# Optimization experiments

Hardware: AMD Instinct MI355X
Metric: run time of the kernel (lower is better)

Reference implementation:

```python
import jax, jax.numpy as jnp
import numpy as np

N_NODES = 50000
N_EDGES = 800000
IN_FEATS = 128
HIDDEN = 128
NUM_CLASSES = 47


def setup_inputs() -> dict:
    key = jax.random.key(0)
    k1, k2, k3, k4 = jax.random.split(key, 4)
    features = jax.random.normal(k1, (N_NODES, IN_FEATS), dtype=jnp.float32)
    edge_index = jax.random.randint(k2, (2, N_EDGES), 0, N_NODES, dtype=jnp.int32)
    # Glorot-style init for weights, zeros for bias (DGL GraphConv defaults)
    W1 = jax.random.normal(k3, (IN_FEATS, HIDDEN), dtype=jnp.float32) * (1.0 / np.sqrt(IN_FEATS))
    b1 = jnp.zeros((HIDDEN,), dtype=jnp.float32)
    W2 = jax.random.normal(k4, (HIDDEN, NUM_CLASSES), dtype=jnp.float32) * (1.0 / np.sqrt(HIDDEN))
    b2 = jnp.zeros((NUM_CLASSES,), dtype=jnp.float32)
    return {"features": features, "edge_index": edge_index,
            "W1": W1, "b1": b1, "W2": W2, "b2": b2}


def _graph_conv(x, W, b, src, dst, norm_src, norm_dst, n_nodes):
    # DGL GraphConv, norm='both': D_dst^{-1/2} A D_src^{-1/2} (X W) + b
    h = (x * norm_src[:, None]) @ W            # transform before aggregation
    agg = jax.ops.segment_sum(h[src], dst, num_segments=n_nodes)
    return agg * norm_dst[:, None] + b


def reference(features, edge_index, W1, b1, W2, b2):
    src, dst = edge_index[0], edge_index[1]
    n = features.shape[0]
    ones = jnp.ones((src.shape[0],), dtype=features.dtype)
    deg_out = jax.ops.segment_sum(ones, src, num_segments=n)
    deg_in = jax.ops.segment_sum(ones, dst, num_segments=n)
    norm_src = jax.lax.rsqrt(jnp.clip(deg_out, 1.0))   # d_out^{-1/2}, clamp >= 1
    norm_dst = jax.lax.rsqrt(jnp.clip(deg_in, 1.0))    # d_in^{-1/2}, clamp >= 1

    h = _graph_conv(features, W1, b1, src, dst, norm_src, norm_dst, n)
    h = jax.nn.relu(h)
    out = _graph_conv(h, W2, b2, src, dst, norm_src, norm_dst, n)
    return out
```

## Files before the change

kernel.cpp:

```cpp
#include <hip/hip_runtime.h>
#include <hip/hip_fp16.h>

#define N_NODES 50000
#define N_EDGES 800000
#define IN_F 128
#define HID 128
#define NCLS 47
#define H2S 48
#define W2C 64
#define NCH 196
#define NB 128
#define CHUNK 6250
#define PDW 12500
#define G1ROWS 256
#define G2ROWS 128


typedef _Float16 f16x8 __attribute__((ext_vector_type(8)));
typedef float f32x4 __attribute__((ext_vector_type(4)));

struct __align__(8)  h2x2 { __half2 a, b; };
struct __align__(16) h2x4 { __half2 a, b, c, d; };

__global__ __launch_bounds__(256) void prep_kernel(const float* __restrict__ W1,
                                                   const float* __restrict__ W2,
                                                   __half* __restrict__ W1Th,
                                                   __half* __restrict__ W1Tl,
                                                   __half* __restrict__ W2Th,
                                                   __half* __restrict__ W2Tl) {
    const int b = blockIdx.x, t = threadIdx.x;
    if (b < 32) {
        const int i0 = b * 512;
        for (int i2 = i0 + t; i2 < i0 + 512; i2 += 256) {
            int cc = i2 >> 7, k = i2 & 127;
            float w = W1[k * HID + cc];
            __half hv = __float2half_rn(w);
            W1Th[i2] = hv;
            W1Tl[i2] = __float2half_rn(w - __half2float(hv));
        }
    } else {
        const int i0 = (b - 32) * 512;
        for (int i2 = i0 + t; i2 < i0 + 512; i2 += 256) {
            int cc = i2 >> 7, k = i2 & 127;
            float w = (cc < NCLS) ? W2[k * NCLS + cc] : 0.f;
            __half hv = __float2half_rn(w);
            W2Th[i2] = hv;
            W2Tl[i2] = __float2half_rn(w - __half2float(hv));
        }
    }
}

__global__ __launch_bounds__(512) void hist_gemm1_kernel(const int* __restrict__ ei,
        unsigned int* __restrict__ Pdst, unsigned int* __restrict__ Psrc,
        const float* __restrict__ X, const __half* __restrict__ W1Th,
        const __half* __restrict__ W1Tl, __half* __restrict__ H1h) {
    __shared__ unsigned int h[PDW];
    const int t = threadIdx.x;
    if (blockIdx.x < 2 * NB) {
        const bool is_src = blockIdx.x >= NB;
        const int chunk = blockIdx.x & (NB - 1);
        const int* ids = is_src ? ei : ei + N_EDGES;
        uint2* h2 = (uint2*)h;
        for (int j = t; j < PDW / 2; j += 512) h2[j] = make_uint2(0u, 0u);
        __syncthreads();
        const int e0 = chunk * CHUNK;
        const int2* e2p = (const int2*)(ids + e0);
        for (int k = t; k < CHUNK / 2; k += 512) {
            int2 v2 = e2p[k];
            atomicAdd(&h[v2.x >> 2], 1u << ((v2.x & 3) * 8));
            atomicAdd(&h[v2.y >> 2], 1u << ((v2.y & 3) * 8));
        }
        __syncthreads();
        unsigned int* P = (is_src ? Psrc : Pdst) + (size_t)chunk * PDW;
        uint2* P2 = (uint2*)P;
        for (int j = t; j < PDW / 2; j += 512) P2[j] = h2[j];
    } else {
        const int lane = t & 63;
        const int wv = t >> 6;
        const int r16 = lane & 15;
        const int kg = lane >> 4;
        const int row0 = (blockIdx.x - 2 * NB) * G1ROWS + wv * 32;
        f32x4 acc[2][8] = {};
#pragma unroll
        for (int s = 0; s < 4; ++s) {
            const int k0 = 32 * s + 8 * kg;
            f16x8 ah[2], al[2];
#pragma unroll
            for (int rt = 0; rt < 2; ++rt) {
                int row = row0 + rt * 16 + r16;
                int rc = row < N_NODES ? row : N_NODES - 1;
                const float4 x0 = *(const float4*)&X[(size_t)rc * IN_F + k0];
                const float4 x1 = *(const float4*)&X[(size_t)rc * IN_F + k0 + 4];
                const float xv[8] = {x0.x, x0.y, x0.z, x0.w,
                                     x1.x, x1.y, x1.z, x1.w};
#pragma unroll
                for (int j = 0; j < 8; ++j) {
                    _Float16 hv = (_Float16)xv[j];
                    ah[rt][j] = hv;
                    al[rt][j] = (_Float16)(xv[j] - (float)hv);
                }
            }
#pragma unroll
            for (int tt = 0; tt < 8; ++tt) {
                const f16x8 bh = *(const f16x8*)&W1Th[(16 * tt + r16) * IN_F + k0];
                const f16x8 bl = *(const f16x8*)&W1Tl[(16 * tt + r16) * IN_F + k0];
#pragma unroll
                for (int rt = 0; rt < 2; ++rt) {
                    acc[rt][tt] = __builtin_amdgcn_mfma_f32_16x16x32_f16(
                        ah[rt], bh, acc[rt][tt], 0, 0, 0);
                    acc[rt][tt] = __builtin_amdgcn_mfma_f32_16x16x32_f16(
                        al[rt], bh, acc[rt][tt], 0, 0, 0);
                    acc[rt][tt] = __builtin_amdgcn_mfma_f32_16x16x32_f16(
                        ah[rt], bl, acc[rt][tt], 0, 0, 0);
                }
            }
        }
#pragma unroll
        for (int rt = 0; rt < 2; ++rt)
#pragma unroll
            for (int j = 0; j < 4; ++j) {
                const int row = row0 + rt * 16 + 4 * kg + j;
                if (row < N_NODES) {
#pragma unroll
                    for (int tt = 0; tt < 8; ++tt)
                        H1h[(size_t)row * HID + 16 * tt + r16] =
                            __float2half_rn(acc[rt][tt][j]);
                }
            }
    }
}

__global__ __launch_bounds__(256) void reduce_kernel(unsigned int* __restrict__ Pdst,
                                                     const unsigned int* __restrict__ Psrc,
                                                     int* __restrict__ cnt_in,
                                                     float* __restrict__ norm_src,
                                                     float* __restrict__ norm_dst,
                                                     int* __restrict__ chunk_sums) {
    __shared__ int sm[256];
    const int t = threadIdx.x;
    const int j = blockIdx.x * 256 + t;
    int tot = 0;
    if (j < PDW) {
        unsigned int run = 0;
#pragma unroll 8
        for (int b = 0; b < NB; ++b) {
            unsigned int v = Pdst[(size_t)b * PDW + j];
            Pdst[(size_t)b * PDW + j] = run;
            run += v;
        }
        int n0 = run & 0xff, n1 = (run >> 8) & 0xff;
        int n2 = (run >> 16) & 0xff, n3 = (run >> 24) & 0xff;
        *(int4*)&cnt_in[4 * j] = make_int4(n0, n1, n2, n3);
        *(float4*)&norm_dst[4 * j] = make_float4(
            rsqrtf(fmaxf((float)n0, 1.0f)), rsqrtf(fmaxf((float)n1, 1.0f)),
            rsqrtf(fmaxf((float)n2, 1.0f)), rsqrtf(fmaxf((float)n3, 1.0f)));
        tot = n0 + n1 + n2 + n3;
        unsigned int rs = 0;
#pragma unroll 8
        for (int b = 0; b < NB; ++b) rs += Psrc[(size_t)b * PDW + j];
        int s0 = rs & 0xff, s1 = (rs >> 8) & 0xff;
        int s2 = (rs >> 16) & 0xff, s3 = (rs >> 24) & 0xff;
        *(float4*)&norm_src[4 * j] = make_float4(
            rsqrtf(fmaxf((float)s0, 1.0f)), rsqrtf(fmaxf((float)s1, 1.0f)),
            rsqrtf(fmaxf((float)s2, 1.0f)), rsqrtf(fmaxf((float)s3, 1.0f)));
    }
    sm[t] = tot;
    __syncthreads();
    const int g = t & 63;
    for (int off = 32; off > 0; off >>= 1) {
        if (g < off) sm[t] += sm[t + off];
        __syncthreads();
    }
    if (g == 0) chunk_sums[blockIdx.x * 4 + (t >> 6)] = sm[t];
}

__global__ __launch_bounds__(256) void scan3_kernel(const int* __restrict__ cnt_in,
                                                    const int* __restrict__ chunk_sums,
                                                    int* __restrict__ offsets) {
    __shared__ int sm[256];
    const int t = threadIdx.x;
    int v = (t < NCH) ? chunk_sums[t] : 0;
    sm[t] = v;
    __syncthreads();
    for (int off = 1; off < 256; off <<= 1) {
        int u = (t >= off) ? sm[t - off] : 0;
        __syncthreads();
        sm[t] += u;
        __syncthreads();
    }
    const int basev = (blockIdx.x == 0) ? 0 : sm[blockIdx.x - 1];
    __syncthreads();
    const int idx = blockIdx.x * 256 + t;
    int c = (idx < N_NODES) ? cnt_in[idx] : 0;
    sm[t] = c;
    __syncthreads();
    for (int off = 1; off < 256; off <<= 1) {
        int u = (t >= off) ? sm[t - off] : 0;
        __syncthreads();
        sm[t] += u;
        __syncthreads();
    }
    if (idx < N_NODES) offsets[idx] = basev + sm[t] - c;
    if (blockIdx.x == 0 && t == 0) offsets[N_NODES] = N_EDGES;
}

__global__ __launch_bounds__(512) void fill_kernel(const int* __restrict__ src,
        const int* __restrict__ dst, const int* __restrict__ offsets,
        const unsigned int* __restrict__ Pdst, int* __restrict__ csr_src) {
    __shared__ __align__(16) unsigned int cur[PDW];
    const int t = threadIdx.x;
    const int chunk = blockIdx.x;
    uint2* c2 = (uint2*)cur;
    for (int j = t; j < PDW / 2; j += 512) c2[j] = make_uint2(0u, 0u);
    __syncthreads();
    const unsigned int* base = Pdst + (size_t)chunk * PDW;
    const int e0 = chunk * CHUNK;
    const int2* d2p = (const int2*)(dst + e0);
    const int2* s2p = (const int2*)(src + e0);
    for (int k = t; k < CHUNK / 2; k += 512) {
        int2 d2 = d2p[k];
        int2 s2 = s2p[k];
        {
            const int d = d2.x;
            const int sh = (d & 3) * 8;
            const unsigned int bw = base[d >> 2];
            const int off = offsets[d];
            unsigned int old = atomicAdd(&cur[d >> 2], 1u << sh);
            csr_src[off + (int)((bw >> sh) & 0xffu) + (int)((old >> sh) & 0xffu)] = s2.x;
        }
        {
            const int d = d2.y;
            const int sh = (d & 3) * 8;
            const unsigned int bw = base[d >> 2];
            const int off = offsets[d];
            unsigned int old = atomicAdd(&cur[d >> 2], 1u << sh);
            csr_src[off + (int)((bw >> sh) & 0xffu) + (int)((old >> sh) & 0xffu)] = s2.y;
        }
    }
}

__global__ __launch_bounds__(256) void gather1_kernel(const __half* __restrict__ H1h,
        const int* __restrict__ offsets, const int* __restrict__ csr_src,
        const float* __restrict__ b1, const float* __restrict__ norm_src,
        const float* __restrict__ norm_dst, __half* __restrict__ Hrelu16) {
    const int lane = threadIdx.x & 63;
    const int q = lane >> 4;
    const int fl = lane & 15;
    const int row = blockIdx.x * 4 + (threadIdx.x >> 6);
    const int beg = offsets[row], end = offsets[row + 1];
    float a0 = 0.f, a1 = 0.f, a2 = 0.f, a3 = 0.f;
    float a4 = 0.f, a5 = 0.f, a6 = 0.f, a7 = 0.f;
    for (int base = beg; base < end; base += 64) {
        int idx = 0;
        float nsv = 0.f;
        if (base + lane < end) {
            idx = csr_src[base + lane];
            nsv = norm_src[idx];
        }
        const int cnt = min(end - base, 64);
        for (int j = 0; j < cnt; j += 16) {
            int e0 = j + q, e1 = j + 4 + q, e2 = j + 8 + q, e3 = j + 12 + q;
            int s0 = __shfl(idx, e0);  float n0 = __shfl(nsv, e0);
            int s1 = __shfl(idx, e1);  float n1 = __shfl(nsv, e1);
            int s2 = __shfl(idx, e2);  float n2 = __shfl(nsv, e2);
            int s3 = __shfl(idx, e3);  float n3 = __shfl(nsv, e3);
            h2x4 v0 = *(const h2x4*)&H1h[(size_t)s0 * HID + 8 * fl];
            h2x4 v1 = *(const h2x4*)&H1h[(size_t)s1 * HID + 8 * fl];
            h2x4 v2 = *(const h2x4*)&H1h[(size_t)s2 * HID + 8 * fl];
            h2x4 v3 = *(const h2x4*)&H1h[(size_t)s3 * HID + 8 * fl];
            float2 f;
            f = __half22float2(v0.a); a0 = fmaf(f.x, n0, a0); a1 = fmaf(f.y, n0, a1);
            f = __half22float2(v0.b); a2 = fmaf(f.x, n0, a2); a3 = fmaf(f.y, n0, a3);
            f = __half22float2(v0.c); a4 = fmaf(f.x, n0, a4); a5 = fmaf(f.y, n0, a5);
            f = __half22float2(v0.d); a6 = fmaf(f.x, n0, a6); a7 = fmaf(f.y, n0, a7);
            f = __half22float2(v1.a); a0 = fmaf(f.x, n1, a0); a1 = fmaf(f.y, n1, a1);
            f = __half22float2(v1.b); a2 = fmaf(f.x, n1, a2); a3 = fmaf(f.y, n1, a3);
            f = __half22float2(v1.c); a4 = fmaf(f.x, n1, a4); a5 = fmaf(f.y, n1, a5);
            f = __half22float2(v1.d); a6 = fmaf(f.x, n1, a6); a7 = fmaf(f.y, n1, a7);
            f = __half22float2(v2.a); a0 = fmaf(f.x, n2, a0); a1 = fmaf(f.y, n2, a1);
            f = __half22float2(v2.b); a2 = fmaf(f.x, n2, a2); a3 = fmaf(f.y, n2, a3);
            f = __half22float2(v2.c); a4 = fmaf(f.x, n2, a4); a5 = fmaf(f.y, n2, a5);
            f = __half22float2(v2.d); a6 = fmaf(f.x, n2, a6); a7 = fmaf(f.y, n2, a7);
            f = __half22float2(v3.a); a0 = fmaf(f.x, n3, a0); a1 = fmaf(f.y, n3, a1);
            f = __half22float2(v3.b); a2 = fmaf(f.x, n3, a2); a3 = fmaf(f.y, n3, a3);
            f = __half22float2(v3.c); a4 = fmaf(f.x, n3, a4); a5 = fmaf(f.y, n3, a5);
            f = __half22float2(v3.d); a6 = fmaf(f.x, n3, a6); a7 = fmaf(f.y, n3, a7);
        }
    }
    a0 += __shfl_xor(a0, 16); a1 += __shfl_xor(a1, 16);
    a2 += __shfl_xor(a2, 16); a3 += __shfl_xor(a3, 16);
    a4 += __shfl_xor(a4, 16); a5 += __shfl_xor(a5, 16);
    a6 += __shfl_xor(a6, 16); a7 += __shfl_xor(a7, 16);
    a0 += __shfl_xor(a0, 32); a1 += __shfl_xor(a1, 32);
    a2 += __shfl_xor(a2, 32); a3 += __shfl_xor(a3, 32);
    a4 += __shfl_xor(a4, 32); a5 += __shfl_xor(a5, 32);
    a6 += __shfl_xor(a6, 32); a7 += __shfl_xor(a7, 32);
    if (lane < 16) {
        float nd = norm_dst[row], ns = norm_src[row];
        float4 bA = *(const float4*)&b1[8 * fl];
        float4 bB = *(const float4*)&b1[8 * fl + 4];
        float o0 = fmaxf(fmaf(a0, nd, bA.x), 0.f) * ns;
        float o1 = fmaxf(fmaf(a1, nd, bA.y), 0.f) * ns;
        float o2 = fmaxf(fmaf(a2, nd, bA.z), 0.f) * ns;
        float o3 = fmaxf(fmaf(a3, nd, bA.w), 0.f) * ns;
        float o4 = fmaxf(fmaf(a4, nd, bB.x), 0.f) * ns;
        float o5 = fmaxf(fmaf(a5, nd, bB.y), 0.f) * ns;
        float o6 = fmaxf(fmaf(a6, nd, bB.z), 0.f) * ns;
        float o7 = fmaxf(fmaf(a7, nd, bB.w), 0.f) * ns;
        h2x4 p = {__floats2half2_rn(o0, o1), __floats2half2_rn(o2, o3),
                  __floats2half2_rn(o4, o5), __floats2half2_rn(o6, o7)};
        *(h2x4*)&Hrelu16[(size_t)row * HID + 8 * fl] = p;
    }
}

__global__ __launch_bounds__(256) void gemm2_kernel(const __half* __restrict__ Hrelu16,
                                                    const __half* __restrict__ W2Th,
                                                    const __half* __restrict__ W2Tl,
                                                    __half* __restrict__ H2h) {
    const int lane = threadIdx.x & 63;
    const int wv = threadIdx.x >> 6;
    const int r16 = lane & 15;
    const int kg = lane >> 4;
    const int row0 = blockIdx.x * G2ROWS + wv * 32;
    f32x4 acc[2][3] = {};
#pragma unroll
    for (int s = 0; s < 4; ++s) {
        const int k0 = 32 * s + 8 * kg;
        f16x8 a[2];
#pragma unroll
        for (int rt = 0; rt < 2; ++rt) {
            int row = row0 + rt * 16 + r16;
            int rc = row < N_NODES ? row : N_NODES - 1;
            a[rt] = *(const f16x8*)&Hrelu16[(size_t)rc * HID + k0];
        }
#pragma unroll
        for (int tt = 0; tt < 3; ++tt) {
            const f16x8 bh = *(const f16x8*)&W2Th[(16 * tt + r16) * HID + k0];
            const f16x8 bl = *(const f16x8*)&W2Tl[(16 * tt + r16) * HID + k0];
#pragma unroll
            for (int rt = 0; rt < 2; ++rt) {
                acc[rt][tt] = __builtin_amdgcn_mfma_f32_16x16x32_f16(
                    a[rt], bh, acc[rt][tt], 0, 0, 0);
                acc[rt][tt] = __builtin_amdgcn_mfma_f32_16x16x32_f16(
                    a[rt], bl, acc[rt][tt], 0, 0, 0);
            }
        }
    }
#pragma unroll
    for (int rt = 0; rt < 2; ++rt)
#pragma unroll
        for (int j = 0; j < 4; ++j) {
            const int row = row0 + rt * 16 + 4 * kg + j;
            if (row < N_NODES) {
#pragma unroll
                for (int tt = 0; tt < 3; ++tt)
                    H2h[(size_t)row * H2S + 16 * tt + r16] =
                        __float2half_rn(acc[rt][tt][j]);
            }
        }
}

__global__ __launch_bounds__(256) void gather2_kernel(const __half* __restrict__ H2h,
        const int* __restrict__ offsets, const int* __restrict__ csr_src,
        const float* __restrict__ b2, const float* __restrict__ norm_dst,
        float* __restrict__ out) {
    const int lane = threadIdx.x & 63;
    const int row = blockIdx.x * 4 + (threadIdx.x >> 6);
    const int beg = offsets[row], end = offsets[row + 1];
    const int cl = min(lane, H2S - 1);
    float acc = 0.f;
    for (int base = beg; base < end; base += 64) {
        int idx = 0;
        float wv = 0.f;
        if (base + lane < end) {
            idx = csr_src[base + lane];
            wv = 1.f;
        }
        const int cnt = min(end - base, 64);
        for (int j = 0; j < cnt; j += 4) {
            int s0 = __shfl(idx, j);     float w0 = __shfl(wv, j);
            int s1 = __shfl(idx, j + 1); float w1 = __shfl(wv, j + 1);
            int s2 = __shfl(idx, j + 2); float w2 = __shfl(wv, j + 2);
            int s3 = __shfl(idx, j + 3); float w3 = __shfl(wv, j + 3);
            float f0 = __half2float(H2h[(size_t)s0 * H2S + cl]);
            float f1 = __half2float(H2h[(size_t)s1 * H2S + cl]);
            float f2 = __half2float(H2h[(size_t)s2 * H2S + cl]);
            float f3 = __half2float(H2h[(size_t)s3 * H2S + cl]);
            acc = fmaf(f0, w0, acc);
            acc = fmaf(f1, w1, acc);
            acc = fmaf(f2, w2, acc);
            acc = fmaf(f3, w3, acc);
        }
    }
    if (lane < NCLS) out[(size_t)row * NCLS + lane] = acc * norm_dst[row] + b2[lane];
}

extern "C" void kernel_launch(void* const* d_in, const int* in_sizes, int n_in,
                              void* d_out, int out_size, void* d_ws, size_t ws_size,
                              hipStream_t stream) {
    const float* X  = (const float*)d_in[0];
    const int*   ei = (const int*)d_in[1];
    const float* W1 = (const float*)d_in[2];
    const float* b1 = (const float*)d_in[3];
    const float* W2 = (const float*)d_in[4];
    const float* b2 = (const float*)d_in[5];
    float* out = (float*)d_out;

    const int* src = ei;
    const int* dst = ei + N_EDGES;

    char* w = (char*)d_ws;
    auto alloc = [&](size_t bytes) {
        char* p = w;
        w += (bytes + 255) & ~(size_t)255;
        return p;
    };
    float*  norm_src   = (float*)alloc(N_NODES * 4);
    float*  norm_dst   = (float*)alloc(N_NODES * 4);
    int*    cnt_in     = (int*)alloc(N_NODES * 4);
    int*    offsets    = (int*)alloc((N_NODES + 1) * 4);
    int*    csr_src    = (int*)alloc((size_t)N_EDGES * 4);
    int*    chunk_sums = (int*)alloc(NCH * 4);
    __half* W1Th       = (__half*)alloc((size_t)IN_F * HID * 2);
    __half* W1Tl       = (__half*)alloc((size_t)IN_F * HID * 2);
    __half* W2Th       = (__half*)alloc((size_t)W2C * HID * 2);
    __half* W2Tl       = (__half*)alloc((size_t)W2C * HID * 2);
    __half* H1h        = (__half*)alloc((size_t)N_NODES * HID * 2);
    __half* Hrelu16    = (__half*)alloc((size_t)N_NODES * HID * 2);
    __half* H2h        = (__half*)alloc((size_t)N_NODES * H2S * 2);
    unsigned int* Pdst = (unsigned int*)alloc((size_t)NB * PDW * 4);
    unsigned int* Psrc = (unsigned int*)alloc((size_t)NB * PDW * 4);

    const int g1_blocks = (N_NODES + G1ROWS - 1) / G1ROWS;
    const int g2_blocks = (N_NODES + G2ROWS - 1) / G2ROWS;
    prep_kernel<<<48, 256, 0, stream>>>(W1, W2, W1Th, W1Tl, W2Th, W2Tl);
    hist_gemm1_kernel<<<2 * NB + g1_blocks, 512, 0, stream>>>(ei, Pdst, Psrc,
                                                              X, W1Th, W1Tl, H1h);
    reduce_kernel<<<(PDW + 255) / 256, 256, 0, stream>>>(Pdst, Psrc, cnt_in,
                                                         norm_src, norm_dst, chunk_sums);
    scan3_kernel<<<NCH, 256, 0, stream>>>(cnt_in, chunk_sums, offsets);
    fill_kernel<<<NB, 512, 0, stream>>>(src, dst, offsets, Pdst, csr_src);
    gather1_kernel<<<N_NODES / 4, 256, 0, stream>>>(H1h, offsets, csr_src, b1,
                                                    norm_src, norm_dst, Hrelu16);
    gemm2_kernel<<<g2_blocks, 256, 0, stream>>>(Hrelu16, W2Th, W2Tl, H2h);
    gather2_kernel<<<N_NODES / 4, 256, 0, stream>>>(H2h, offsets, csr_src, b2,
                                                    norm_dst, out);
}
```

Baseline: 207.2 us.

## Fuse all pipeline stages into one cooperative persistent kernel with grid syncs

Replaces the eight separate kernel launches with a single cooperative mega-kernel that runs each stage as a grid-strided job loop, separated by grid.sync(). The aim is to remove per-launch overhead and inter-kernel gaps. The grid is capped at 512 blocks of 512 threads, so stages that used to launch tens of thousands of small blocks now loop. It also moves the gemm1 stage after the histogram stage, so the two no longer overlap. The trade-offs are grid-wide barrier cost, parallelism limited by occupancy, and the 50KB LDS array shared by every stage, which may limit blocks per CU.

```diff
diff --git a/kernel.cpp b/kernel.cpp
--- a/kernel.cpp
+++ b/kernel.cpp
@@ -1,5 +1,8 @@
 #include <hip/hip_runtime.h>
 #include <hip/hip_fp16.h>
+#include <hip/hip_cooperative_groups.h>
+
+namespace cg = cooperative_groups;
 
 #define N_NODES 50000
 #define N_EDGES 800000
@@ -13,7 +16,9 @@
 #define CHUNK 6250
 #define PDW 12500
 #define G1ROWS 256
-#define G2ROWS 128
+#define G2ROWS 256
+#define NTHR 512
+#define MAXG 512
 
 
 typedef _Float16 f16x8 __attribute__((ext_vector_type(8)));
@@ -22,96 +27,333 @@
 struct __align__(8)  h2x2 { __half2 a, b; };
 struct __align__(16) h2x4 { __half2 a, b, c, d; };
 
-__global__ __launch_bounds__(256) void prep_kernel(const float* __restrict__ W1,
-                                                   const float* __restrict__ W2,
-                                                   __half* __restrict__ W1Th,
-                                                   __half* __restrict__ W1Tl,
-                                                   __half* __restrict__ W2Th,
-                                                   __half* __restrict__ W2Tl) {
-    const int b = blockIdx.x, t = threadIdx.x;
-    if (b < 32) {
-        const int i0 = b * 512;
-        for (int i2 = i0 + t; i2 < i0 + 512; i2 += 256) {
-            int cc = i2 >> 7, k = i2 & 127;
-            float w = W1[k * HID + cc];
-            __half hv = __float2half_rn(w);
-            W1Th[i2] = hv;
-            W1Tl[i2] = __float2half_rn(w - __half2float(hv));
-        }
-    } else {
-        const int i0 = (b - 32) * 512;
-        for (int i2 = i0 + t; i2 < i0 + 512; i2 += 256) {
-            int cc = i2 >> 7, k = i2 & 127;
-            float w = (cc < NCLS) ? W2[k * NCLS + cc] : 0.f;
-            __half hv = __float2half_rn(w);
-            W2Th[i2] = hv;
-            W2Tl[i2] = __float2half_rn(w - __half2float(hv));
-        }
-    }
-}
-
-__global__ __launch_bounds__(512) void hist_gemm1_kernel(const int* __restrict__ ei,
-        unsigned int* __restrict__ Pdst, unsigned int* __restrict__ Psrc,
-        const float* __restrict__ X, const __half* __restrict__ W1Th,
-        const __half* __restrict__ W1Tl, __half* __restrict__ H1h) {
-    __shared__ unsigned int h[PDW];
+__global__ __launch_bounds__(NTHR, 4) void mega_kernel(
+    const float* __restrict__ X, const int* __restrict__ ei,
+    const float* __restrict__ W1, const float* __restrict__ b1,
+    const float* __restrict__ W2, const float* __restrict__ b2,
+    float* __restrict__ out,
+    float* __restrict__ norm_src, float* __restrict__ norm_dst,
+    int* __restrict__ cnt_in, int* __restrict__ offsets,
+    int* __restrict__ csr_src, int* __restrict__ chunk_sums,
+    __half* __restrict__ W1Th, __half* __restrict__ W1Tl,
+    __half* __restrict__ W2Th, __half* __restrict__ W2Tl,
+    __half* __restrict__ H1h, __half* __restrict__ Hrelu16,
+    __half* __restrict__ H2h,
+    unsigned int* __restrict__ Pdst, unsigned int* __restrict__ Psrc)
+{
+    cg::grid_group grid = cg::this_grid();
+    __shared__ __align__(16) unsigned int lds[PDW];
     const int t = threadIdx.x;
-    if (blockIdx.x < 2 * NB) {
-        const bool is_src = blockIdx.x >= NB;
-        const int chunk = blockIdx.x & (NB - 1);
-        const int* ids = is_src ? ei : ei + N_EDGES;
-        uint2* h2 = (uint2*)h;
-        for (int j = t; j < PDW / 2; j += 512) h2[j] = make_uint2(0u, 0u);
+    const int G = gridDim.x;
+    const int lane = t & 63;
+    const int* srcp = ei;
+    const int* dstp = ei + N_EDGES;
+
+    for (int job = blockIdx.x; job < 2 * NB + 48; job += G) {
+        if (job < 2 * NB) {
+            const bool is_src = job >= NB;
+            const int chunk = job & (NB - 1);
+            const int* ids = is_src ? srcp : dstp;
+            uint2* h2 = (uint2*)lds;
+            for (int j = t; j < PDW / 2; j += NTHR) h2[j] = make_uint2(0u, 0u);
+            __syncthreads();
+            const int e0 = chunk * CHUNK;
+            const int2* e2p = (const int2*)(ids + e0);
+            for (int k = t; k < CHUNK / 2; k += NTHR) {
+                int2 v2 = e2p[k];
+                atomicAdd(&lds[v2.x >> 2], 1u << ((v2.x & 3) * 8));
+                atomicAdd(&lds[v2.y >> 2], 1u << ((v2.y & 3) * 8));
+            }
+            __syncthreads();
+            unsigned int* P = (is_src ? Psrc : Pdst) + (size_t)chunk * PDW;
+            uint2* P2 = (uint2*)P;
+            for (int j = t; j < PDW / 2; j += NTHR) P2[j] = h2[j];
+            __syncthreads();
+        } else {
+            const int pj = job - 2 * NB;
+            if (pj < 32) {
+                const int i0 = pj * 512;
+                for (int i2 = i0 + t; i2 < i0 + 512; i2 += NTHR) {
+                    int cc = i2 >> 7, k = i2 & 127;
+                    float w = W1[k * HID + cc];
+                    __half hv = __float2half_rn(w);
+                    W1Th[i2] = hv;
+                    W1Tl[i2] = __float2half_rn(w - __half2float(hv));
+                }
+            } else {
+                const int i0 = (pj - 32) * 512;
+                for (int i2 = i0 + t; i2 < i0 + 512; i2 += NTHR) {
+                    int cc = i2 >> 7, k = i2 & 127;
+                    float w = (cc < NCLS) ? W2[k * NCLS + cc] : 0.f;
+                    __half hv = __float2half_rn(w);
+                    W2Th[i2] = hv;
+                    W2Tl[i2] = __float2half_rn(w - __half2float(hv));
+                }
+            }
+        }
+    }
+    grid.sync();
+
+    for (int job = blockIdx.x; job < 221; job += G) {
+        if (job < 196) {
+            const int wv = t >> 6;
+            const int r16 = lane & 15;
+            const int kg = lane >> 4;
+            const int row0 = job * G1ROWS + wv * 32;
+            f32x4 acc[2][8] = {};
+#pragma unroll
+            for (int s = 0; s < 4; ++s) {
+                const int k0 = 32 * s + 8 * kg;
+                f16x8 ah[2], al[2];
+#pragma unroll
+                for (int rt = 0; rt < 2; ++rt) {
+                    int row = row0 + rt * 16 + r16;
+                    int rc = row < N_NODES ? row : N_NODES - 1;
+                    const float4 x0 = *(const float4*)&X[(size_t)rc * IN_F + k0];
+                    const float4 x1 = *(const float4*)&X[(size_t)rc * IN_F + k0 + 4];
+                    const float xv[8] = {x0.x, x0.y, x0.z, x0.w,
+                                         x1.x, x1.y, x1.z, x1.w};
+#pragma unroll
+                    for (int j = 0; j < 8; ++j) {
+                        _Float16 hv = (_Float16)xv[j];
+                        ah[rt][j] = hv;
+                        al[rt][j] = (_Float16)(xv[j] - (float)hv);
+                    }
+                }
+#pragma unroll
+                for (int tt = 0; tt < 8; ++tt) {
+                    const f16x8 bh = *(const f16x8*)&W1Th[(16 * tt + r16) * IN_F + k0];
+                    const f16x8 bl = *(const f16x8*)&W1Tl[(16 * tt + r16) * IN_F + k0];
+#pragma unroll
+                    for (int rt = 0; rt < 2; ++rt) {
+                        acc[rt][tt] = __builtin_amdgcn_mfma_f32_16x16x32_f16(
+                            ah[rt], bh, acc[rt][tt], 0, 0, 0);
+                        acc[rt][tt] = __builtin_amdgcn_mfma_f32_16x16x32_f16(
+                            al[rt], bh, acc[rt][tt], 0, 0, 0);
+                        acc[rt][tt] = __builtin_amdgcn_mfma_f32_16x16x32_f16(
+                            ah[rt], bl, acc[rt][tt], 0, 0, 0);
+                    }
+                }
+            }
+#pragma unroll
+            for (int rt = 0; rt < 2; ++rt)
+#pragma unroll
+                for (int j = 0; j < 4; ++j) {
+                    const int row = row0 + rt * 16 + 4 * kg + j;
+                    if (row < N_NODES) {
+#pragma unroll
+                        for (int tt = 0; tt < 8; ++tt)
+                            H1h[(size_t)row * HID + 16 * tt + r16] =
+                                __float2half_rn(acc[rt][tt][j]);
+                    }
+                }
+        } else {
+            int* sm = (int*)lds;
+            const int v = 2 * (job - 196) + (t >> 8);
+            const int tl = t & 255;
+            const int j = v * 256 + tl;
+            int tot = 0;
+            if (j < PDW) {
+                unsigned int run = 0;
+#pragma unroll 8
+                for (int bb = 0; bb < NB; ++bb) {
+                    unsigned int vv = Pdst[(size_t)bb * PDW + j];
+                    Pdst[(size_t)bb * PDW + j] = run;
+                    run += vv;
+                }
+                int n0 = run & 0xff, n1 = (run >> 8) & 0xff;
+                int n2 = (run >> 16) & 0xff, n3 = (run >> 24) & 0xff;
+                *(int4*)&cnt_in[4 * j] = make_int4(n0, n1, n2, n3);
+                *(float4*)&norm_dst[4 * j] = make_float4(
+                    rsqrtf(fmaxf((float)n0, 1.0f)), rsqrtf(fmaxf((float)n1, 1.0f)),
+                    rsqrtf(fmaxf((float)n2, 1.0f)), rsqrtf(fmaxf((float)n3, 1.0f)));
+                tot = n0 + n1 + n2 + n3;
+                unsigned int rs = 0;
+#pragma unroll 8
+                for (int bb = 0; bb < NB; ++bb) rs += Psrc[(size_t)bb * PDW + j];
+                int s0 = rs & 0xff, s1 = (rs >> 8) & 0xff;
+                int s2 = (rs >> 16) & 0xff, s3 = (rs >> 24) & 0xff;
+                *(float4*)&norm_src[4 * j] = make_float4(
+                    rsqrtf(fmaxf((float)s0, 1.0f)), rsqrtf(fmaxf((float)s1, 1.0f)),
+                    rsqrtf(fmaxf((float)s2, 1.0f)), rsqrtf(fmaxf((float)s3, 1.0f)));
+            }
+            sm[t] = tot;
+            __syncthreads();
+            for (int off = 32; off > 0; off >>= 1) {
+                if ((t & 63) < off) sm[t] += sm[t + off];
+                __syncthreads();
+            }
+            if ((t & 63) == 0) {
+                int ci = v * 4 + (tl >> 6);
+                if (ci < NCH) chunk_sums[ci] = sm[t];
+            }
+            __syncthreads();
+        }
+    }
+    grid.sync();
+
+    for (int job = blockIdx.x; job < 98; job += G) {
+        int* smc = (int*)lds;
+        int* smn = (int*)lds + 256;
+        if (t < 256) smc[t] = (t < NCH) ? chunk_sums[t] : 0;
         __syncthreads();
+        for (int off = 1; off < 256; off <<= 1) {
+            int u = 0;
+            if (t < 256 && t >= off) u = smc[t - off];
+            __syncthreads();
+            if (t < 256) smc[t] += u;
+            __syncthreads();
+        }
+        const int v = 2 * job + (t >> 8);
+        const int tl = t & 255;
+        const int basev = (v == 0) ? 0 : smc[v - 1];
+        const int idx = v * 256 + tl;
+        int c = (idx < N_NODES) ? cnt_in[idx] : 0;
+        smn[t] = c;
+        __syncthreads();
+        for (int off = 1; off < 256; off <<= 1) {
+            int u = (tl >= off) ? smn[t - off] : 0;
+            __syncthreads();
+            smn[t] += u;
+            __syncthreads();
+        }
+        if (idx < N_NODES) offsets[idx] = basev + smn[t] - c;
+        if (job == 0 && t == 0) offsets[N_NODES] = N_EDGES;
+        __syncthreads();
+    }
+    grid.sync();
+
+    for (int chunk = blockIdx.x; chunk < NB; chunk += G) {
+        uint2* c2 = (uint2*)lds;
+        for (int j = t; j < PDW / 2; j += NTHR) c2[j] = make_uint2(0u, 0u);
+        __syncthreads();
+        const unsigned int* base = Pdst + (size_t)chunk * PDW;
         const int e0 = chunk * CHUNK;
-        const int2* e2p = (const int2*)(ids + e0);
-        for (int k = t; k < CHUNK / 2; k += 512) {
-            int2 v2 = e2p[k];
-            atomicAdd(&h[v2.x >> 2], 1u << ((v2.x & 3) * 8));
-            atomicAdd(&h[v2.y >> 2], 1u << ((v2.y & 3) * 8));
+        const int2* d2p = (const int2*)(dstp + e0);
+        const int2* s2p = (const int2*)(srcp + e0);
+        for (int k = t; k < CHUNK / 2; k += NTHR) {
+            int2 d2 = d2p[k];
+            int2 s2 = s2p[k];
+            {
+                const int d = d2.x;
+                const int sh = (d & 3) * 8;
+                const unsigned int bw = base[d >> 2];
+                const int off = offsets[d];
+                unsigned int old = atomicAdd(&lds[d >> 2], 1u << sh);
+                csr_src[off + (int)((bw >> sh) & 0xffu) + (int)((old >> sh) & 0xffu)] = s2.x;
+            }
+            {
+                const int d = d2.y;
+                const int sh = (d & 3) * 8;
+                const unsigned int bw = base[d >> 2];
+                const int off = offsets[d];
+                unsigned int old = atomicAdd(&lds[d >> 2], 1u << sh);
+                csr_src[off + (int)((bw >> sh) & 0xffu) + (int)((old >> sh) & 0xffu)] = s2.y;
+            }
         }
         __syncthreads();
-        unsigned int* P = (is_src ? Psrc : Pdst) + (size_t)chunk * PDW;
-        uint2* P2 = (uint2*)P;
-        for (int j = t; j < PDW / 2; j += 512) P2[j] = h2[j];
-    } else {
-        const int lane = t & 63;
+    }
+    grid.sync();
+
+    {
+        const int q = lane >> 4;
+        const int fl = lane & 15;
+        for (int r0 = blockIdx.x * 8; r0 < N_NODES; r0 += G * 8) {
+            const int row = r0 + (t >> 6);
+            const int beg = offsets[row], end = offsets[row + 1];
+            float a0 = 0.f, a1 = 0.f, a2 = 0.f, a3 = 0.f;
+            float a4 = 0.f, a5 = 0.f, a6 = 0.f, a7 = 0.f;
+            for (int base = beg; base < end; base += 64) {
+                int idx = 0;
+                float nsv = 0.f;
+                if (base + lane < end) {
+                    idx = csr_src[base + lane];
+                    nsv = norm_src[idx];
+                }
+                const int cnt = min(end - base, 64);
+                for (int j = 0; j < cnt; j += 16) {
+                    int e0 = j + q, e1 = j + 4 + q, e2 = j + 8 + q, e3 = j + 12 + q;
+                    int s0 = __shfl(idx, e0);  float n0 = __shfl(nsv, e0);
+                    int s1 = __shfl(idx, e1);  float n1 = __shfl(nsv, e1);
+                    int s2 = __shfl(idx, e2);  float n2 = __shfl(nsv, e2);
+                    int s3 = __shfl(idx, e3);  float n3 = __shfl(nsv, e3);
+                    h2x4 v0 = *(const h2x4*)&H1h[(size_t)s0 * HID + 8 * fl];
+                    h2x4 v1 = *(const h2x4*)&H1h[(size_t)s1 * HID + 8 * fl];
+                    h2x4 v2 = *(const h2x4*)&H1h[(size_t)s2 * HID + 8 * fl];
+                    h2x4 v3 = *(const h2x4*)&H1h[(size_t)s3 * HID + 8 * fl];
+                    float2 f;
+                    f = __half22float2(v0.a); a0 = fmaf(f.x, n0, a0); a1 = fmaf(f.y, n0, a1);
+                    f = __half22float2(v0.b); a2 = fmaf(f.x, n0, a2); a3 = fmaf(f.y, n0, a3);
+                    f = __half22float2(v0.c); a4 = fmaf(f.x, n0, a4); a5 = fmaf(f.y, n0, a5);
+                    f = __half22float2(v0.d); a6 = fmaf(f.x, n0, a6); a7 = fmaf(f.y, n0, a7);
+                    f = __half22float2(v1.a); a0 = fmaf(f.x, n1, a0); a1 = fmaf(f.y, n1, a1);
+                    f = __half22float2(v1.b); a2 = fmaf(f.x, n1, a2); a3 = fmaf(f.y, n1, a3);
+                    f = __half22float2(v1.c); a4 = fmaf(f.x, n1, a4); a5 = fmaf(f.y, n1, a5);
+                    f = __half22float2(v1.d); a6 = fmaf(f.x, n1, a6); a7 = fmaf(f.y, n1, a7);
+                    f = __half22float2(v2.a); a0 = fmaf(f.x, n2, a0); a1 = fmaf(f.y, n2, a1);
+                    f = __half22float2(v2.b); a2 = fmaf(f.x, n2, a2); a3 = fmaf(f.y, n2, a3);
+                    f = __half22float2(v2.c); a4 = fmaf(f.x, n2, a4); a5 = fmaf(f.y, n2, a5);
+                    f = __half22float2(v2.d); a6 = fmaf(f.x, n2, a6); a7 = fmaf(f.y, n2, a7);
+                    f = __half22float2(v3.a); a0 = fmaf(f.x, n3, a0); a1 = fmaf(f.y, n3, a1);
+                    f = __half22float2(v3.b); a2 = fmaf(f.x, n3, a2); a3 = fmaf(f.y, n3, a3);
+                    f = __half22float2(v3.c); a4 = fmaf(f.x, n3, a4); a5 = fmaf(f.y, n3, a5);
+                    f = __half22float2(v3.d); a6 = fmaf(f.x, n3, a6); a7 = fmaf(f.y, n3, a7);
+                }
+            }
+            a0 += __shfl_xor(a0, 16); a1 += __shfl_xor(a1, 16);
+            a2 += __shfl_xor(a2, 16); a3 += __shfl_xor(a3, 16);
+            a4 += __shfl_xor(a4, 16); a5 += __shfl_xor(a5, 16);
+            a6 += __shfl_xor(a6, 16); a7 += __shfl_xor(a7, 16);
+            a0 += __shfl_xor(a0, 32); a1 += __shfl_xor(a1, 32);
+            a2 += __shfl_xor(a2, 32); a3 += __shfl_xor(a3, 32);
+            a4 += __shfl_xor(a4, 32); a5 += __shfl_xor(a5, 32);
+            a6 += __shfl_xor(a6, 32); a7 += __shfl_xor(a7, 32);
+            if (lane < 16) {
+                float nd = norm_dst[row], ns = norm_src[row];
+                float4 bA = *(const float4*)&b1[8 * fl];
+                float4 bB = *(const float4*)&b1[8 * fl + 4];
+                float o0 = fmaxf(fmaf(a0, nd, bA.x), 0.f) * ns;
+                float o1 = fmaxf(fmaf(a1, nd, bA.y), 0.f) * ns;
+                float o2 = fmaxf(fmaf(a2, nd, bA.z), 0.f) * ns;
+                float o3 = fmaxf(fmaf(a3, nd, bA.w), 0.f) * ns;
+                float o4 = fmaxf(fmaf(a4, nd, bB.x), 0.f) * ns;
+                float o5 = fmaxf(fmaf(a5, nd, bB.y), 0.f) * ns;
+                float o6 = fmaxf(fmaf(a6, nd, bB.z), 0.f) * ns;
+                float o7 = fmaxf(fmaf(a7, nd, bB.w), 0.f) * ns;
+                h2x4 p = {__floats2half2_rn(o0, o1), __floats2half2_rn(o2, o3),
+                          __floats2half2_rn(o4, o5), __floats2half2_rn(o6, o7)};
+                *(h2x4*)&Hrelu16[(size_t)row * HID + 8 * fl] = p;
+            }
+        }
+    }
+    grid.sync();
+
+    for (int job = blockIdx.x; job < 196; job += G) {
         const int wv = t >> 6;
         const int r16 = lane & 15;
         const int kg = lane >> 4;
-        const int row0 = (blockIdx.x - 2 * NB) * G1ROWS + wv * 32;
-        f32x4 acc[2][8] = {};
+        const int row0 = job * G2ROWS + wv * 32;
+        f32x4 acc[2][3] = {};
 #pragma unroll
         for (int s = 0; s < 4; ++s) {
             const int k0 = 32 * s + 8 * kg;
-            f16x8 ah[2], al[2];
+            f16x8 a[2];
 #pragma unroll
             for (int rt = 0; rt < 2; ++rt) {
                 int row = row0 + rt * 16 + r16;
                 int rc = row < N_NODES ? row : N_NODES - 1;
-                const float4 x0 = *(const float4*)&X[(size_t)rc * IN_F + k0];
-                const float4 x1 = *(const float4*)&X[(size_t)rc * IN_F + k0 + 4];
-                const float xv[8] = {x0.x, x0.y, x0.z, x0.w,
-                                     x1.x, x1.y, x1.z, x1.w};
-#pragma unroll
-                for (int j = 0; j < 8; ++j) {
-                    _Float16 hv = (_Float16)xv[j];
-                    ah[rt][j] = hv;
-                    al[rt][j] = (_Float16)(xv[j] - (float)hv);
-                }
-            }
-#pragma unroll
-            for (int tt = 0; tt < 8; ++tt) {
-                const f16x8 bh = *(const f16x8*)&W1Th[(16 * tt + r16) * IN_F + k0];
-                const f16x8 bl = *(const f16x8*)&W1Tl[(16 * tt + r16) * IN_F + k0];
+                a[rt] = *(const f16x8*)&Hrelu16[(size_t)rc * HID + k0];
+            }
+#pragma unroll
+            for (int tt = 0; tt < 3; ++tt) {
+                const f16x8 bh = *(const f16x8*)&W2Th[(16 * tt + r16) * HID + k0];
+                const f16x8 bl = *(const f16x8*)&W2Tl[(16 * tt + r16) * HID + k0];
 #pragma unroll
                 for (int rt = 0; rt < 2; ++rt) {
                     acc[rt][tt] = __builtin_amdgcn_mfma_f32_16x16x32_f16(
-                        ah[rt], bh, acc[rt][tt], 0, 0, 0);
+                        a[rt], bh, acc[rt][tt], 0, 0, 0);
                     acc[rt][tt] = __builtin_amdgcn_mfma_f32_16x16x32_f16(
-                        al[rt], bh, acc[rt][tt], 0, 0, 0);
-                    acc[rt][tt] = __builtin_amdgcn_mfma_f32_16x16x32_f16(
-                        ah[rt], bl, acc[rt][tt], 0, 0, 0);
+                        a[rt], bl, acc[rt][tt], 0, 0, 0);
                 }
             }
         }
@@ -122,277 +364,46 @@
                 const int row = row0 + rt * 16 + 4 * kg + j;
                 if (row < N_NODES) {
 #pragma unroll
-                    for (int tt = 0; tt < 8; ++tt)
-                        H1h[(size_t)row * HID + 16 * tt + r16] =
+                    for (int tt = 0; tt < 3; ++tt)
+                        H2h[(size_t)row * H2S + 16 * tt + r16] =
                             __float2half_rn(acc[rt][tt][j]);
                 }
             }
     }
-}
-
-__global__ __launch_bounds__(256) void reduce_kernel(unsigned int* __restrict__ Pdst,
-                                                     const unsigned int* __restrict__ Psrc,
-                                                     int* __restrict__ cnt_in,
-                                                     float* __restrict__ norm_src,
-                                                     float* __restrict__ norm_dst,
-                                                     int* __restrict__ chunk_sums) {
-    __shared__ int sm[256];
-    const int t = threadIdx.x;
-    const int j = blockIdx.x * 256 + t;
-    int tot = 0;
-    if (j < PDW) {
-        unsigned int run = 0;
-#pragma unroll 8
-        for (int b = 0; b < NB; ++b) {
-            unsigned int v = Pdst[(size_t)b * PDW + j];
-            Pdst[(size_t)b * PDW + j] = run;
-            run += v;
-        }
-        int n0 = run & 0xff, n1 = (run >> 8) & 0xff;
-        int n2 = (run >> 16) & 0xff, n3 = (run >> 24) & 0xff;
-        *(int4*)&cnt_in[4 * j] = make_int4(n0, n1, n2, n3);
-        *(float4*)&norm_dst[4 * j] = make_float4(
-            rsqrtf(fmaxf((float)n0, 1.0f)), rsqrtf(fmaxf((float)n1, 1.0f)),
-            rsqrtf(fmaxf((float)n2, 1.0f)), rsqrtf(fmaxf((float)n3, 1.0f)));
-        tot = n0 + n1 + n2 + n3;
-        unsigned int rs = 0;
-#pragma unroll 8
-        for (int b = 0; b < NB; ++b) rs += Psrc[(size_t)b * PDW + j];
-        int s0 = rs & 0xff, s1 = (rs >> 8) & 0xff;
-        int s2 = (rs >> 16) & 0xff, s3 = (rs >> 24) & 0xff;
-        *(float4*)&norm_src[4 * j] = make_float4(
-            rsqrtf(fmaxf((float)s0, 1.0f)), rsqrtf(fmaxf((float)s1, 1.0f)),
-            rsqrtf(fmaxf((float)s2, 1.0f)), rsqrtf(fmaxf((float)s3, 1.0f)));
-    }
-    sm[t] = tot;
-    __syncthreads();
-    const int g = t & 63;
-    for (int off = 32; off > 0; off >>= 1) {
-        if (g < off) sm[t] += sm[t + off];
-        __syncthreads();
-    }
-    if (g == 0) chunk_sums[blockIdx.x * 4 + (t >> 6)] = sm[t];
-}
-
-__global__ __launch_bounds__(256) void scan3_kernel(const int* __restrict__ cnt_in,
-                                                    const int* __restrict__ chunk_sums,
-                                                    int* __restrict__ offsets) {
-    __shared__ int sm[256];
-    const int t = threadIdx.x;
-    int v = (t < NCH) ? chunk_sums[t] : 0;
-    sm[t] = v;
-    __syncthreads();
-    for (int off = 1; off < 256; off <<= 1) {
-        int u = (t >= off) ? sm[t - off] : 0;
-        __syncthreads();
-        sm[t] += u;
-        __syncthreads();
-    }
-    const int basev = (blockIdx.x == 0) ? 0 : sm[blockIdx.x - 1];
-    __syncthreads();
-    const int idx = blockIdx.x * 256 + t;
-    int c = (idx < N_NODES) ? cnt_in[idx] : 0;
-    sm[t] = c;
-    __syncthreads();
-    for (int off = 1; off < 256; off <<= 1) {
-        int u = (t >= off) ? sm[t - off] : 0;
-        __syncthreads();
-        sm[t] += u;
-        __syncthreads();
-    }
-    if (idx < N_NODES) offsets[idx] = basev + sm[t] - c;
-    if (blockIdx.x == 0 && t == 0) offsets[N_NODES] = N_EDGES;
-}
-
-__global__ __launch_bounds__(512) void fill_kernel(const int* __restrict__ src,
-        const int* __restrict__ dst, const int* __restrict__ offsets,
-        const unsigned int* __restrict__ Pdst, int* __restrict__ csr_src) {
-    __shared__ __align__(16) unsigned int cur[PDW];
-    const int t = threadIdx.x;
-    const int chunk = blockIdx.x;
-    uint2* c2 = (uint2*)cur;
-    for (int j = t; j < PDW / 2; j += 512) c2[j] = make_uint2(0u, 0u);
-    __syncthreads();
-    const unsigned int* base = Pdst + (size_t)chunk * PDW;
-    const int e0 = chunk * CHUNK;
-    const int2* d2p = (const int2*)(dst + e0);
-    const int2* s2p = (const int2*)(src + e0);
-    for (int k = t; k < CHUNK / 2; k += 512) {
-        int2 d2 = d2p[k];
-        int2 s2 = s2p[k];
-        {
-            const int d = d2.x;
-            const int sh = (d & 3) * 8;
-            const unsigned int bw = base[d >> 2];
-            const int off = offsets[d];
-            unsigned int old = atomicAdd(&cur[d >> 2], 1u << sh);
-            csr_src[off + (int)((bw >> sh) & 0xffu) + (int)((old >> sh) & 0xffu)] = s2.x;
-        }
-        {
-            const int d = d2.y;
-            const int sh = (d & 3) * 8;
-            const unsigned int bw = base[d >> 2];
-            const int off = offsets[d];
-            unsigned int old = atomicAdd(&cur[d >> 2], 1u << sh);
-            csr_src[off + (int)((bw >> sh) & 0xffu) + (int)((old >> sh) & 0xffu)] = s2.y;
-        }
-    }
-}
-
-__global__ __launch_bounds__(256) void gather1_kernel(const __half* __restrict__ H1h,
-        const int* __restrict__ offsets, const int* __restrict__ csr_src,
-        const float* __restrict__ b1, const float* __restrict__ norm_src,
-        const float* __restrict__ norm_dst, __half* __restrict__ Hrelu16) {
-    const int lane = threadIdx.x & 63;
-    const int q = lane >> 4;
-    const int fl = lane & 15;
-    const int row = blockIdx.x * 4 + (threadIdx.x >> 6);
-    const int beg = offsets[row], end = offsets[row + 1];
-    float a0 = 0.f, a1 = 0.f, a2 = 0.f, a3 = 0.f;
-    float a4 = 0.f, a5 = 0.f, a6 = 0.f, a7 = 0.f;
-    for (int base = beg; base < end; base += 64) {
-        int idx = 0;
-        float nsv = 0.f;
-        if (base + lane < end) {
-            idx = csr_src[base + lane];
-            nsv = norm_src[idx];
-        }
-        const int cnt = min(end - base, 64);
-        for (int j = 0; j < cnt; j += 16) {
-            int e0 = j + q, e1 = j + 4 + q, e2 = j + 8 + q, e3 = j + 12 + q;
-            int s0 = __shfl(idx, e0);  float n0 = __shfl(nsv, e0);
-            int s1 = __shfl(idx, e1);  float n1 = __shfl(nsv, e1);
-            int s2 = __shfl(idx, e2);  float n2 = __shfl(nsv, e2);
-            int s3 = __shfl(idx, e3);  float n3 = __shfl(nsv, e3);
-            h2x4 v0 = *(const h2x4*)&H1h[(size_t)s0 * HID + 8 * fl];
-            h2x4 v1 = *(const h2x4*)&H1h[(size_t)s1 * HID + 8 * fl];
-            h2x4 v2 = *(const h2x4*)&H1h[(size_t)s2 * HID + 8 * fl];
-            h2x4 v3 = *(const h2x4*)&H1h[(size_t)s3 * HID + 8 * fl];
-            float2 f;
-            f = __half22float2(v0.a); a0 = fmaf(f.x, n0, a0); a1 = fmaf(f.y, n0, a1);
-            f = __half22float2(v0.b); a2 = fmaf(f.x, n0, a2); a3 = fmaf(f.y, n0, a3);
-            f = __half22float2(v0.c); a4 = fmaf(f.x, n0, a4); a5 = fmaf(f.y, n0, a5);
-            f = __half22float2(v0.d); a6 = fmaf(f.x, n0, a6); a7 = fmaf(f.y, n0, a7);
-            f = __half22float2(v1.a); a0 = fmaf(f.x, n1, a0); a1 = fmaf(f.y, n1, a1);
-            f = __half22float2(v1.b); a2 = fmaf(f.x, n1, a2); a3 = fmaf(f.y, n1, a3);
-            f = __half22float2(v1.c); a4 = fmaf(f.x, n1, a4); a5 = fmaf(f.y, n1, a5);
-            f = __half22float2(v1.d); a6 = fmaf(f.x, n1, a6); a7 = fmaf(f.y, n1, a7);
-            f = __half22float2(v2.a); a0 = fmaf(f.x, n2, a0); a1 = fmaf(f.y, n2, a1);
-            f = __half22float2(v2.b); a2 = fmaf(f.x, n2, a2); a3 = fmaf(f.y, n2, a3);
-            f = __half22float2(v2.c); a4 = fmaf(f.x, n2, a4); a5 = fmaf(f.y, n2, a5);
-            f = __half22float2(v2.d); a6 = fmaf(f.x, n2, a6); a7 = fmaf(f.y, n2, a7);
-            f = __half22float2(v3.a); a0 = fmaf(f.x, n3, a0); a1 = fmaf(f.y, n3, a1);
-            f = __half22float2(v3.b); a2 = fmaf(f.x, n3, a2); a3 = fmaf(f.y, n3, a3);
-            f = __half22float2(v3.c); a4 = fmaf(f.x, n3, a4); a5 = fmaf(f.y, n3, a5);
-            f = __half22float2(v3.d); a6 = fmaf(f.x, n3, a6); a7 = fmaf(f.y, n3, a7);
-        }
-    }
-    a0 += __shfl_xor(a0, 16); a1 += __shfl_xor(a1, 16);
-    a2 += __shfl_xor(a2, 16); a3 += __shfl_xor(a3, 16);
-    a4 += __shfl_xor(a4, 16); a5 += __shfl_xor(a5, 16);
-    a6 += __shfl_xor(a6, 16); a7 += __shfl_xor(a7, 16);
-    a0 += __shfl_xor(a0, 32); a1 += __shfl_xor(a1, 32);
-    a2 += __shfl_xor(a2, 32); a3 += __shfl_xor(a3, 32);
-    a4 += __shfl_xor(a4, 32); a5 += __shfl_xor(a5, 32);
-    a6 += __shfl_xor(a6, 32); a7 += __shfl_xor(a7, 32);
-    if (lane < 16) {
-        float nd = norm_dst[row], ns = norm_src[row];
-        float4 bA = *(const float4*)&b1[8 * fl];
-        float4 bB = *(const float4*)&b1[8 * fl + 4];
-        float o0 = fmaxf(fmaf(a0, nd, bA.x), 0.f) * ns;
-        float o1 = fmaxf(fmaf(a1, nd, bA.y), 0.f) * ns;
-        float o2 = fmaxf(fmaf(a2, nd, bA.z), 0.f) * ns;
-        float o3 = fmaxf(fmaf(a3, nd, bA.w), 0.f) * ns;
-        float o4 = fmaxf(fmaf(a4, nd, bB.x), 0.f) * ns;
-        float o5 = fmaxf(fmaf(a5, nd, bB.y), 0.f) * ns;
-        float o6 = fmaxf(fmaf(a6, nd, bB.z), 0.f) * ns;
-        float o7 = fmaxf(fmaf(a7, nd, bB.w), 0.f) * ns;
-        h2x4 p = {__floats2half2_rn(o0, o1), __floats2half2_rn(o2, o3),
-                  __floats2half2_rn(o4, o5), __floats2half2_rn(o6, o7)};
-        *(h2x4*)&Hrelu16[(size_t)row * HID + 8 * fl] = p;
-    }
-}
-
-__global__ __launch_bounds__(256) void gemm2_kernel(const __half* __restrict__ Hrelu16,
-                                                    const __half* __restrict__ W2Th,
-                                                    const __half* __restrict__ W2Tl,
-                                                    __half* __restrict__ H2h) {
-    const int lane = threadIdx.x & 63;
-    const int wv = threadIdx.x >> 6;
-    const int r16 = lane & 15;
-    const int kg = lane >> 4;
-    const int row0 = blockIdx.x * G2ROWS + wv * 32;
-    f32x4 acc[2][3] = {};
-#pragma unroll
-    for (int s = 0; s < 4; ++s) {
-        const int k0 = 32 * s + 8 * kg;
-        f16x8 a[2];
-#pragma unroll
-        for (int rt = 0; rt < 2; ++rt) {
-            int row = row0 + rt * 16 + r16;
-            int rc = row < N_NODES ? row : N_NODES - 1;
-            a[rt] = *(const f16x8*)&Hrelu16[(size_t)rc * HID + k0];
-        }
-#pragma unroll
-        for (int tt = 0; tt < 3; ++tt) {
-            const f16x8 bh = *(const f16x8*)&W2Th[(16 * tt + r16) * HID + k0];
-            const f16x8 bl = *(const f16x8*)&W2Tl[(16 * tt + r16) * HID + k0];
-#pragma unroll
-            for (int rt = 0; rt < 2; ++rt) {
-                acc[rt][tt] = __builtin_amdgcn_mfma_f32_16x16x32_f16(
-                    a[rt], bh, acc[rt][tt], 0, 0, 0);
-                acc[rt][tt] = __builtin_amdgcn_mfma_f32_16x16x32_f16(
-                    a[rt], bl, acc[rt][tt], 0, 0, 0);
-            }
-        }
-    }
-#pragma unroll
-    for (int rt = 0; rt < 2; ++rt)
-#pragma unroll
-        for (int j = 0; j < 4; ++j) {
-            const int row = row0 + rt * 16 + 4 * kg + j;
-            if (row < N_NODES) {
-#pragma unroll
-                for (int tt = 0; tt < 3; ++tt)
-                    H2h[(size_t)row * H2S + 16 * tt + r16] =
-                        __float2half_rn(acc[rt][tt][j]);
-            }
-        }
-}
-
-__global__ __launch_bounds__(256) void gather2_kernel(const __half* __restrict__ H2h,
-        const int* __restrict__ offsets, const int* __restrict__ csr_src,
-        const float* __restrict__ b2, const float* __restrict__ norm_dst,
-        float* __restrict__ out) {
-    const int lane = threadIdx.x & 63;
-    const int row = blockIdx.x * 4 + (threadIdx.x >> 6);
-    const int beg = offsets[row], end = offsets[row + 1];
-    const int cl = min(lane, H2S - 1);
-    float acc = 0.f;
-    for (int base = beg; base < end; base += 64) {
-        int idx = 0;
-        float wv = 0.f;
-        if (base + lane < end) {
-            idx = csr_src[base + lane];
-            wv = 1.f;
-        }
-        const int cnt = min(end - base, 64);
-        for (int j = 0; j < cnt; j += 4) {
-            int s0 = __shfl(idx, j);     float w0 = __shfl(wv, j);
-            int s1 = __shfl(idx, j + 1); float w1 = __shfl(wv, j + 1);
-            int s2 = __shfl(idx, j + 2); float w2 = __shfl(wv, j + 2);
-            int s3 = __shfl(idx, j + 3); float w3 = __shfl(wv, j + 3);
-            float f0 = __half2float(H2h[(size_t)s0 * H2S + cl]);
-            float f1 = __half2float(H2h[(size_t)s1 * H2S + cl]);
-            float f2 = __half2float(H2h[(size_t)s2 * H2S + cl]);
-            float f3 = __half2float(H2h[(size_t)s3 * H2S + cl]);
-            acc = fmaf(f0, w0, acc);
-            acc = fmaf(f1, w1, acc);
-            acc = fmaf(f2, w2, acc);
-            acc = fmaf(f3, w3, acc);
-        }
-    }
-    if (lane < NCLS) out[(size_t)row * NCLS + lane] = acc * norm_dst[row] + b2[lane];
+    grid.sync();
+
+    {
+        const int cl = min(lane, H2S - 1);
+        for (int r0 = blockIdx.x * 8; r0 < N_NODES; r0 += G * 8) {
+            const int row = r0 + (t >> 6);
+            const int beg = offsets[row], end = offsets[row + 1];
+            float acc = 0.f;
+            for (int base = beg; base < end; base += 64) {
+                int idx = 0;
+                float wv = 0.f;
+                if (base + lane < end) {
+                    idx = csr_src[base + lane];
+                    wv = 1.f;
+                }
+                const int cnt = min(end - base, 64);
+                for (int j = 0; j < cnt; j += 4) {
+                    int s0 = __shfl(idx, j);     float w0 = __shfl(wv, j);
+                    int s1 = __shfl(idx, j + 1); float w1 = __shfl(wv, j + 1);
+                    int s2 = __shfl(idx, j + 2); float w2 = __shfl(wv, j + 2);
+                    int s3 = __shfl(idx, j + 3); float w3 = __shfl(wv, j + 3);
+                    float f0 = __half2float(H2h[(size_t)s0 * H2S + cl]);
+                    float f1 = __half2float(H2h[(size_t)s1 * H2S + cl]);
+                    float f2 = __half2float(H2h[(size_t)s2 * H2S + cl]);
+                    float f3 = __half2float(H2h[(size_t)s3 * H2S + cl]);
+                    acc = fmaf(f0, w0, acc);
+                    acc = fmaf(f1, w1, acc);
+                    acc = fmaf(f2, w2, acc);
+                    acc = fmaf(f3, w3, acc);
+                }
+            }
+            if (lane < NCLS) out[(size_t)row * NCLS + lane] = acc * norm_dst[row] + b2[lane];
+        }
+    }
 }
 
 extern "C" void kernel_launch(void* const* d_in, const int* in_sizes, int n_in,
@@ -405,9 +416,6 @@
     const float* W2 = (const float*)d_in[4];
     const float* b2 = (const float*)d_in[5];
     float* out = (float*)d_out;
-
-    const int* src = ei;
-    const int* dst = ei + N_EDGES;
 
     char* w = (char*)d_ws;
     auto alloc = [&](size_t bytes) {
@@ -431,18 +439,18 @@
     unsigned int* Pdst = (unsigned int*)alloc((size_t)NB * PDW * 4);
     unsigned int* Psrc = (unsigned int*)alloc((size_t)NB * PDW * 4);
 
-    const int g1_blocks = (N_NODES + G1ROWS - 1) / G1ROWS;
-    const int g2_blocks = (N_NODES + G2ROWS - 1) / G2ROWS;
-    prep_kernel<<<48, 256, 0, stream>>>(W1, W2, W1Th, W1Tl, W2Th, W2Tl);
-    hist_gemm1_kernel<<<2 * NB + g1_blocks, 512, 0, stream>>>(ei, Pdst, Psrc,
-                                                              X, W1Th, W1Tl, H1h);
-    reduce_kernel<<<(PDW + 255) / 256, 256, 0, stream>>>(Pdst, Psrc, cnt_in,
-                                                         norm_src, norm_dst, chunk_sums);
-    scan3_kernel<<<NCH, 256, 0, stream>>>(cnt_in, chunk_sums, offsets);
-    fill_kernel<<<NB, 512, 0, stream>>>(src, dst, offsets, Pdst, csr_src);
-    gather1_kernel<<<N_NODES / 4, 256, 0, stream>>>(H1h, offsets, csr_src, b1,
-                                                    norm_src, norm_dst, Hrelu16);
-    gemm2_kernel<<<g2_blocks, 256, 0, stream>>>(Hrelu16, W2Th, W2Tl, H2h);
-    gather2_kernel<<<N_NODES / 4, 256, 0, stream>>>(H2h, offsets, csr_src, b2,
-                                                    norm_dst, out);
+    int maxActive = 0;
+    hipOccupancyMaxActiveBlocksPerMultiprocessor(&maxActive, mega_kernel, NTHR, 0);
+    if (maxActive < 1) maxActive = 1;
+    long long Gl = (long long)maxActive * 256;
+    int G = (Gl > MAXG) ? MAXG : (int)Gl;
+
+    void* args[] = {
+        (void*)&X, (void*)&ei, (void*)&W1, (void*)&b1, (void*)&W2, (void*)&b2,
+        (void*)&out, (void*)&norm_src, (void*)&norm_dst, (void*)&cnt_in,
+        (void*)&offsets, (void*)&csr_src, (void*)&chunk_sums,
+        (void*)&W1Th, (void*)&W1Tl, (void*)&W2Th, (void*)&W2Tl,
+        (void*)&H1h, (void*)&Hrelu16, (void*)&H2h, (void*)&Pdst, (void*)&Psrc };
+    hipLaunchCooperativeKernel((void*)mega_kernel, dim3(G), dim3(NTHR),
+                               args, 0, stream);
 }
```

After: 482.1 us. 133% more time.
